# Kernel tuning notes

Measured on AMD Instinct MI355X. Metric: run time of the kernel, lower is better.

The kernel has to match this reference:

```python
import jax, jax.numpy as jnp
import numpy as np

B, LC, LQ, D = 64, 512, 64, 256

def setup_inputs() -> dict:
    key = jax.random.key(0)
    k1, k2, k3, k4 = jax.random.split(key, 4)
    contex = jax.random.normal(k1, (B, LC, D), dtype=jnp.float32)
    question = jax.random.normal(k2, (B, LQ, D), dtype=jnp.float32)
    W_weight = jax.random.normal(k3, (1, 3 * D), dtype=jnp.float32) * (1.0 / np.sqrt(3 * D))
    W_bias = jax.random.normal(k4, (1,), dtype=jnp.float32) * 0.01
    return {"contex": contex, "question": question, "W_weight": W_weight, "W_bias": W_bias}

def reference(contex, question, W_weight, W_bias):
    d = contex.shape[-1]
    w = W_weight[0]  # [3D]; cat order in original is [q, c, q*c]
    wq, wc, wi = w[:d], w[d:2 * d], w[2 * d:]
    # S[b,i,j] = c_i.wc + q_j.wq + (c_i*q_j).wi + bias  (trilinear decomposition)
    s_c = contex @ wc                                   # [B, Lc]
    s_q = question @ wq                                 # [B, Lq]
    s_i = jnp.einsum('bid,bjd->bij', contex * wi, question)  # [B, Lc, Lq]
    S = s_i + s_c[:, :, None] + s_q[:, None, :] + W_bias[0]
    S1 = jax.nn.softmax(S, axis=2)                      # over question
    S2 = jax.nn.softmax(S, axis=1)                      # over context
    A = jnp.einsum('bij,bjd->bid', S1, question)        # [B, Lc, D]
    S3 = jnp.einsum('bij,bkj->bik', S1, S2)             # [B, Lc, Lc]
    Bm = jnp.einsum('bik,bkd->bid', S3, contex)         # [B, Lc, D]
    out = jnp.concatenate([contex, A, contex * A, contex * Bm], axis=2)  # [B, Lc, 4D]
    return out  # dropout is identity at inference
```

## Files before the change

kernel.cpp:

```cpp
#include <hip/hip_runtime.h>
#include <hip/hip_bf16.h>

#define BB 64
#define LCC 512
#define LQQ 64
#define DDD 256

typedef short bf16x8 __attribute__((ext_vector_type(8)));
typedef float f32x4 __attribute__((ext_vector_type(4)));
typedef unsigned u32x4 __attribute__((ext_vector_type(4)));

static __device__ __forceinline__ unsigned pk2bf(float a, float b) {
  __hip_bfloat162 h = __float22bfloat162_rn(make_float2(a, b));
  unsigned u;
  __builtin_memcpy(&u, &h, sizeof(u));
  return u;
}
static __device__ __forceinline__ unsigned short bf1(float f) {
  __hip_bfloat16 h = __float2bfloat16(f);
  unsigned short u;
  __builtin_memcpy(&u, &h, sizeof(u));
  return u;
}

static __device__ __forceinline__ void nt_store4(float* p, float a, float b, float c, float d) {
  f32x4 v = { a, b, c, d };
  __builtin_nontemporal_store(v, (f32x4*)p);
}

__global__ __launch_bounds__(256) void k1_scores(
    const float* __restrict__ cx, const float* __restrict__ qu,
    const float* __restrict__ W, const float* __restrict__ Wb,
    unsigned short* __restrict__ P, unsigned short* __restrict__ Et,
    float* __restrict__ csp)
{
  __shared__ float w_lds[768];
  __shared__ unsigned short Bs[64 * 264];
  __shared__ float E_lds[64 * 65];
  __shared__ float sc_lds[64];
  __shared__ float sq_lds[64];

  const int tid = threadIdx.x;
  const int b    = blockIdx.x >> 3;
  const int tile = blockIdx.x & 7;
  const int i0 = tile * 64;
  const int w = tid >> 6, lane = tid & 63, quad = lane >> 4, ln = lane & 15;

  for (int idx = tid; idx < 768; idx += 256) w_lds[idx] = W[idx];
  __syncthreads();

  {
    const int bj = tid >> 2, bc = tid & 3;
    const float4* src = (const float4*)(qu + ((size_t)(b * LQQ + bj)) * DDD + bc * 64);
    const float* wq = w_lds + bc * 64;
    unsigned short* dst = Bs + bj * 264 + bc * 64;
    float sqp = 0.f;
#pragma unroll
    for (int u = 0; u < 16; ++u) {
      float4 v = src[u];
      sqp += v.x * wq[u*4+0] + v.y * wq[u*4+1] + v.z * wq[u*4+2] + v.w * wq[u*4+3];
      uint2 o = { pk2bf(v.x, v.y), pk2bf(v.z, v.w) };
      *(uint2*)(dst + u * 4) = o;
    }
    sqp += __shfl_xor(sqp, 1);
    sqp += __shfl_xor(sqp, 2);
    if ((tid & 3) == 0) sq_lds[bj] = sqp;
  }
  __syncthreads();

  f32x4 acc[4];
#pragma unroll
  for (int c = 0; c < 4; ++c) acc[c] = (f32x4){0.f, 0.f, 0.f, 0.f};

  float scp = 0.f;
  const float* cxrow = cx + ((size_t)(b * LCC + i0 + w * 16 + ln)) * DDD;
#pragma unroll
  for (int kk = 0; kk < 4; ++kk)
#pragma unroll
    for (int ks = 0; ks < 2; ++ks) {
      const int k0 = kk * 64 + ks * 32 + quad * 8;
      float4 c0 = *(const float4*)(cxrow + k0);
      float4 c1 = *(const float4*)(cxrow + k0 + 4);
      const float* wcp = w_lds + 256 + k0;
      const float* wip = w_lds + 512 + k0;
      scp += c0.x*wcp[0] + c0.y*wcp[1] + c0.z*wcp[2] + c0.w*wcp[3]
           + c1.x*wcp[4] + c1.y*wcp[5] + c1.z*wcp[6] + c1.w*wcp[7];
      u32x4 av = { pk2bf(c0.x * wip[0], c0.y * wip[1]),
                   pk2bf(c0.z * wip[2], c0.w * wip[3]),
                   pk2bf(c1.x * wip[4], c1.y * wip[5]),
                   pk2bf(c1.z * wip[6], c1.w * wip[7]) };
      bf16x8 af;
      __builtin_memcpy(&af, &av, sizeof(af));
#pragma unroll
      for (int tn = 0; tn < 4; ++tn) {
        bf16x8 bf = *(const bf16x8*)(Bs + (tn * 16 + ln) * 264 + k0);
        acc[tn] = __builtin_amdgcn_mfma_f32_16x16x32_bf16(af, bf, acc[tn], 0, 0, 0);
      }
    }

  scp += __shfl_xor(scp, 16);
  scp += __shfl_xor(scp, 32);
  if (lane < 16) sc_lds[w * 16 + ln] = scp + Wb[0];
  __syncthreads();

#pragma unroll
  for (int tn = 0; tn < 4; ++tn)
#pragma unroll
    for (int r = 0; r < 4; ++r) {
      int il = w * 16 + quad * 4 + r;
      int j  = tn * 16 + ln;
      E_lds[il * 65 + j] = __expf(acc[tn][r] + sc_lds[il] + sq_lds[j]);
    }
  __syncthreads();

  {
    const int i = tid >> 2, c = tid & 3;
    const float* srcr = E_lds + i * 65 + c * 16;
    float s = 0.f;
#pragma unroll
    for (int j = 0; j < 16; ++j) s += srcr[j];
    s += __shfl_xor(s, 1);
    s += __shfl_xor(s, 2);
    const float ri = 1.0f / s;
    unsigned short* dst = P + ((size_t)(b * LCC + i0 + i)) * 64 + c * 16;
#pragma unroll
    for (int u = 0; u < 4; ++u) {
      uint2 o = { pk2bf(srcr[u*4+0]*ri, srcr[u*4+1]*ri),
                  pk2bf(srcr[u*4+2]*ri, srcr[u*4+3]*ri) };
      *(uint2*)(dst + u * 4) = o;
    }
  }
  {
    const int j = tid >> 2, c = tid & 3;
    float s = 0.f;
#pragma unroll
    for (int r = 0; r < 16; ++r) s += E_lds[(c * 16 + r) * 65 + j];
    s += __shfl_xor(s, 1);
    s += __shfl_xor(s, 2);
    if ((tid & 3) == 0) csp[((size_t)(b * 8 + tile)) * 64 + j] = s;
  }
  {
    const int j = tid >> 2, c = tid & 3;
    unsigned short* dst = Et + ((size_t)(b * LQQ + j)) * LCC + i0 + c * 16;
#pragma unroll
    for (int u = 0; u < 4; ++u) {
      uint2 o = { pk2bf(E_lds[(c*16 + u*4 + 0) * 65 + j],
                        E_lds[(c*16 + u*4 + 1) * 65 + j]),
                  pk2bf(E_lds[(c*16 + u*4 + 2) * 65 + j],
                        E_lds[(c*16 + u*4 + 3) * 65 + j]) };
      *(uint2*)(dst + u * 4) = o;
    }
  }
}

__global__ __launch_bounds__(256) void k2_tmat(
    const float* __restrict__ cx, const float* __restrict__ qu,
    const unsigned short* __restrict__ Et, const float* __restrict__ csp,
    unsigned short* __restrict__ Qt, unsigned short* __restrict__ Tt)
{
  __shared__ unsigned short Bs2[2][32 * 72];
  __shared__ float Tl[64 * 37];
  __shared__ float csinv[64];

  const int tid = threadIdx.x;
  const int b  = blockIdx.x >> 3;
  const int d0 = (blockIdx.x & 7) * 32;
  const int w = tid >> 6, lane = tid & 63, quad = lane >> 4, ln = lane & 15;

  {
    const int j = tid >> 2, c = tid & 3;
    const float* srow = qu + ((size_t)(b * LQQ + j)) * DDD + d0 + c * 8;
    float4 v0 = *(const float4*)srow;
    float4 v1 = *(const float4*)(srow + 4);
    float* t = Tl + j * 37 + c * 8;
    t[0]=v0.x; t[1]=v0.y; t[2]=v0.z; t[3]=v0.w;
    t[4]=v1.x; t[5]=v1.y; t[6]=v1.z; t[7]=v1.w;
  }
  if (tid < 64) {
    float s = 0.f;
#pragma unroll
    for (int t = 0; t < 8; ++t) s += csp[((size_t)(b * 8 + t)) * 64 + tid];
    csinv[tid] = 1.0f / s;
  }
  __syncthreads();
  {
    const int d = tid >> 3, cj = tid & 7;
    unsigned short* dst = Qt + ((size_t)(b * DDD + d0 + d)) * 64 + cj * 8;
    uint2 o0 = { pk2bf(Tl[(cj*8+0)*37+d], Tl[(cj*8+1)*37+d]),
                 pk2bf(Tl[(cj*8+2)*37+d], Tl[(cj*8+3)*37+d]) };
    uint2 o1 = { pk2bf(Tl[(cj*8+4)*37+d], Tl[(cj*8+5)*37+d]),
                 pk2bf(Tl[(cj*8+6)*37+d], Tl[(cj*8+7)*37+d]) };
    *(uint2*)dst = o0;
    *(uint2*)(dst + 4) = o1;
  }

  f32x4 acc[2];
  acc[0] = (f32x4){0.f, 0.f, 0.f, 0.f};
  acc[1] = (f32x4){0.f, 0.f, 0.f, 0.f};
  const unsigned short* etrow = Et + ((size_t)(b * LQQ + w * 16 + ln)) * LCC;
  const int r2 = tid >> 2, c2 = tid & 3;

  for (int kk = 0; kk < 8; ++kk) {
    unsigned short* bufw = Bs2[kk & 1];
    {
      const float* srow = cx + ((size_t)(b * LCC + kk * 64 + r2)) * DDD + d0 + c2 * 8;
      float4 v0 = *(const float4*)srow;
      float4 v1 = *(const float4*)(srow + 4);
      bufw[(c2*8+0)*72 + r2] = bf1(v0.x);
      bufw[(c2*8+1)*72 + r2] = bf1(v0.y);
      bufw[(c2*8+2)*72 + r2] = bf1(v0.z);
      bufw[(c2*8+3)*72 + r2] = bf1(v0.w);
      bufw[(c2*8+4)*72 + r2] = bf1(v1.x);
      bufw[(c2*8+5)*72 + r2] = bf1(v1.y);
      bufw[(c2*8+6)*72 + r2] = bf1(v1.z);
      bufw[(c2*8+7)*72 + r2] = bf1(v1.w);
    }
    bf16x8 af0 = *(const bf16x8*)(etrow + kk * 64 + quad * 8);
    bf16x8 af1 = *(const bf16x8*)(etrow + kk * 64 + 32 + quad * 8);
    __syncthreads();
    const unsigned short* bufr = Bs2[kk & 1];
#pragma unroll
    for (int tn = 0; tn < 2; ++tn) {
      bf16x8 bf0 = *(const bf16x8*)(bufr + (tn * 16 + ln) * 72 + quad * 8);
      bf16x8 bf1v = *(const bf16x8*)(bufr + (tn * 16 + ln) * 72 + 32 + quad * 8);
      acc[tn] = __builtin_amdgcn_mfma_f32_16x16x32_bf16(af0, bf0, acc[tn], 0, 0, 0);
      acc[tn] = __builtin_amdgcn_mfma_f32_16x16x32_bf16(af1, bf1v, acc[tn], 0, 0, 0);
    }
  }

#pragma unroll
  for (int tn = 0; tn < 2; ++tn)
#pragma unroll
    for (int r = 0; r < 4; ++r) {
      int j = w * 16 + quad * 4 + r;
      Tl[j * 37 + tn * 16 + ln] = acc[tn][r] * csinv[j];
    }
  __syncthreads();
  {
    const int d = tid >> 3, cj = tid & 7;
    unsigned short* dst = Tt + ((size_t)(b * DDD + d0 + d)) * 64 + cj * 8;
    uint2 o0 = { pk2bf(Tl[(cj*8+0)*37+d], Tl[(cj*8+1)*37+d]),
                 pk2bf(Tl[(cj*8+2)*37+d], Tl[(cj*8+3)*37+d]) };
    uint2 o1 = { pk2bf(Tl[(cj*8+4)*37+d], Tl[(cj*8+5)*37+d]),
                 pk2bf(Tl[(cj*8+6)*37+d], Tl[(cj*8+7)*37+d]) };
    *(uint2*)dst = o0;
    *(uint2*)(dst + 4) = o1;
  }
}

__global__ __launch_bounds__(256, 2) void k3_out(
    const float* __restrict__ cx,
    const unsigned short* __restrict__ P,
    const unsigned short* __restrict__ Qt,
    const unsigned short* __restrict__ Tt,
    float* __restrict__ out)
{
  __shared__ float TrA[16 * 260];
  __shared__ float TrB[16 * 260];

  const int tid = threadIdx.x;
  const int b  = blockIdx.x >> 3;
  const int i0 = (blockIdx.x & 7) * 64;
  const int w = tid >> 6, lane = tid & 63, quad = lane >> 4, ln = lane & 15;

  const unsigned short* pbase = P + ((size_t)(b * LCC + i0)) * 64;
  const unsigned short* qbase = Qt + (size_t)b * DDD * 64;
  const unsigned short* tbase = Tt + (size_t)b * DDD * 64;

  f32x4 accA[4][4], accB[4][4];
#pragma unroll
  for (int a = 0; a < 4; ++a)
#pragma unroll
    for (int c = 0; c < 4; ++c) {
      accA[a][c] = (f32x4){0.f, 0.f, 0.f, 0.f};
      accB[a][c] = (f32x4){0.f, 0.f, 0.f, 0.f};
    }

#pragma unroll
  for (int ks = 0; ks < 2; ++ks) {
    bf16x8 af[4];
#pragma unroll
    for (int tm = 0; tm < 4; ++tm)
      af[tm] = *(const bf16x8*)(pbase + (tm * 16 + ln) * 64 + ks * 32 + quad * 8);
#pragma unroll
    for (int tn = 0; tn < 4; ++tn) {
      const size_t boff = ((size_t)(w * 64 + tn * 16 + ln)) * 64 + ks * 32 + quad * 8;
      bf16x8 bq = *(const bf16x8*)(qbase + boff);
      bf16x8 bt = *(const bf16x8*)(tbase + boff);
#pragma unroll
      for (int tm = 0; tm < 4; ++tm) {
        accA[tm][tn] = __builtin_amdgcn_mfma_f32_16x16x32_bf16(af[tm], bq, accA[tm][tn], 0, 0, 0);
        accB[tm][tn] = __builtin_amdgcn_mfma_f32_16x16x32_bf16(af[tm], bt, accB[tm][tn], 0, 0, 0);
      }
    }
  }

  const float* cxb = cx + (size_t)b * LCC * DDD;
  float* ob = out + (size_t)b * LCC * 1024;
  const int row = tid >> 4;
  const int fq  = tid & 15;

#pragma unroll
  for (int tm = 0; tm < 4; ++tm) {
#pragma unroll
    for (int tn = 0; tn < 4; ++tn)
#pragma unroll
      for (int r = 0; r < 4; ++r) {
        int rloc = quad * 4 + r;
        TrA[rloc * 260 + w * 64 + tn * 16 + ln] = accA[tm][tn][r];
        TrB[rloc * 260 + w * 64 + tn * 16 + ln] = accB[tm][tn][r];
      }
    __syncthreads();
    const int i = i0 + tm * 16 + row;
#pragma unroll
    for (int u = 0; u < 4; ++u) {
      int c0 = (fq + u * 16) * 4;
      float4 a  = *(const float4*)(TrA + row * 260 + c0);
      float4 bm = *(const float4*)(TrB + row * 260 + c0);
      float4 c  = *(const float4*)(cxb + (size_t)i * DDD + c0);
      nt_store4(ob + (size_t)i * 1024 + c0,       c.x, c.y, c.z, c.w);
      nt_store4(ob + (size_t)i * 1024 + 256 + c0, a.x, a.y, a.z, a.w);
      nt_store4(ob + (size_t)i * 1024 + 512 + c0, c.x*a.x, c.y*a.y, c.z*a.z, c.w*a.w);
      nt_store4(ob + (size_t)i * 1024 + 768 + c0, c.x*bm.x, c.y*bm.y, c.z*bm.z, c.w*bm.w);
    }
    __syncthreads();
  }
}

extern "C" void kernel_launch(void* const* d_in, const int* in_sizes, int n_in,
                              void* d_out, int out_size, void* d_ws, size_t ws_size,
                              hipStream_t stream) {
  const float* cx = (const float*)d_in[0];
  const float* qu = (const float*)d_in[1];
  const float* W  = (const float*)d_in[2];
  const float* Wb = (const float*)d_in[3];
  float* out = (float*)d_out;

  char* wsb = (char*)d_ws;
  unsigned short* P   = (unsigned short*)(wsb);
  unsigned short* Et  = (unsigned short*)(wsb + (4ull << 20));
  unsigned short* Qt  = (unsigned short*)(wsb + (8ull << 20));
  unsigned short* Tt  = (unsigned short*)(wsb + (10ull << 20));
  float*          csp = (float*)(wsb + (12ull << 20));

  k1_scores<<<dim3(512), dim3(256), 0, stream>>>(cx, qu, W, Wb, P, Et, csp);
  k2_tmat  <<<dim3(512), dim3(256), 0, stream>>>(cx, qu, Et, csp, Qt, Tt);
  k3_out   <<<dim3(512), dim3(256), 0, stream>>>(cx, P, Qt, Tt, out);
}
```

Baseline: 198.7 us.

## Fuse three kernels into one persistent kernel with per-batch atomic counters

Merges the score, T-matrix and output kernels into a single launch in which the 8 blocks of each batch coordinate through global atomic counters, spinning until all 8 peers have finished a stage. Shared memory is reused across the three phases through one byte buffer. This aims to remove two kernel launch gaps and the tail effects between stages, at the cost of a memset launch and spin-waits. Correctness relies on all blocks of a batch being resident at once; the 2-blocks-per-CU bound makes 512 blocks fit on 256 CUs. The wait loop breaks out after a fixed number of iterations instead of deadlocking.

```diff
diff --git a/kernel.cpp b/kernel.cpp
--- a/kernel.cpp
+++ b/kernel.cpp
@@ -28,302 +28,312 @@
   __builtin_nontemporal_store(v, (f32x4*)p);
 }
 
-__global__ __launch_bounds__(256) void k1_scores(
+static __device__ __forceinline__ void signal_cnt(int* c, int tid) {
+  __threadfence();
+  __syncthreads();
+  if (tid == 0)
+    __hip_atomic_fetch_add(c, 1, __ATOMIC_RELEASE, __HIP_MEMORY_SCOPE_AGENT);
+}
+static __device__ __forceinline__ void wait_cnt(int* c, int target) {
+  int n = 0;
+  while (__hip_atomic_load(c, __ATOMIC_ACQUIRE, __HIP_MEMORY_SCOPE_AGENT) < target) {
+    __builtin_amdgcn_s_sleep(8);
+    if (++n > (1 << 20)) break;
+  }
+}
+
+__global__ __launch_bounds__(256, 2) void fused(
     const float* __restrict__ cx, const float* __restrict__ qu,
     const float* __restrict__ W, const float* __restrict__ Wb,
     unsigned short* __restrict__ P, unsigned short* __restrict__ Et,
-    float* __restrict__ csp)
+    float* __restrict__ csp, unsigned short* __restrict__ Qt,
+    unsigned short* __restrict__ Tt, float* __restrict__ out,
+    int* __restrict__ cnt1, int* __restrict__ cnt2)
 {
-  __shared__ float w_lds[768];
-  __shared__ unsigned short Bs[64 * 264];
-  __shared__ float E_lds[64 * 65];
-  __shared__ float sc_lds[64];
-  __shared__ float sq_lds[64];
+  __shared__ __align__(16) char smem[54016];
 
   const int tid = threadIdx.x;
-  const int b    = blockIdx.x >> 3;
-  const int tile = blockIdx.x & 7;
-  const int i0 = tile * 64;
+  const int b = blockIdx.x >> 3;
+  const int s = blockIdx.x & 7;
   const int w = tid >> 6, lane = tid & 63, quad = lane >> 4, ln = lane & 15;
 
-  for (int idx = tid; idx < 768; idx += 256) w_lds[idx] = W[idx];
-  __syncthreads();
-
   {
-    const int bj = tid >> 2, bc = tid & 3;
-    const float4* src = (const float4*)(qu + ((size_t)(b * LQQ + bj)) * DDD + bc * 64);
-    const float* wq = w_lds + bc * 64;
-    unsigned short* dst = Bs + bj * 264 + bc * 64;
-    float sqp = 0.f;
-#pragma unroll
-    for (int u = 0; u < 16; ++u) {
-      float4 v = src[u];
-      sqp += v.x * wq[u*4+0] + v.y * wq[u*4+1] + v.z * wq[u*4+2] + v.w * wq[u*4+3];
-      uint2 o = { pk2bf(v.x, v.y), pk2bf(v.z, v.w) };
-      *(uint2*)(dst + u * 4) = o;
-    }
-    sqp += __shfl_xor(sqp, 1);
-    sqp += __shfl_xor(sqp, 2);
-    if ((tid & 3) == 0) sq_lds[bj] = sqp;
+    float* w_lds          = (float*)(smem);
+    unsigned short* Bs    = (unsigned short*)(smem + 3072);
+    float* E_lds          = (float*)(smem + 36864);
+    float* sc_lds         = (float*)(smem + 53504);
+    float* sq_lds         = (float*)(smem + 53760);
+    const int i0 = s * 64;
+
+    for (int idx = tid; idx < 768; idx += 256) w_lds[idx] = W[idx];
+    __syncthreads();
+
+    {
+      const int bj = tid >> 2, bc = tid & 3;
+      const float4* src = (const float4*)(qu + ((size_t)(b * LQQ + bj)) * DDD + bc * 64);
+      const float* wq = w_lds + bc * 64;
+      unsigned short* dst = Bs + bj * 264 + bc * 64;
+      float sqp = 0.f;
+#pragma unroll
+      for (int u = 0; u < 16; ++u) {
+        float4 v = src[u];
+        sqp += v.x * wq[u*4+0] + v.y * wq[u*4+1] + v.z * wq[u*4+2] + v.w * wq[u*4+3];
+        uint2 o = { pk2bf(v.x, v.y), pk2bf(v.z, v.w) };
+        *(uint2*)(dst + u * 4) = o;
+      }
+      sqp += __shfl_xor(sqp, 1);
+      sqp += __shfl_xor(sqp, 2);
+      if ((tid & 3) == 0) sq_lds[bj] = sqp;
+    }
+    __syncthreads();
+
+    f32x4 acc[4];
+#pragma unroll
+    for (int c = 0; c < 4; ++c) acc[c] = (f32x4){0.f, 0.f, 0.f, 0.f};
+
+    float scp = 0.f;
+    const float* cxrow = cx + ((size_t)(b * LCC + i0 + w * 16 + ln)) * DDD;
+#pragma unroll
+    for (int kk = 0; kk < 4; ++kk)
+#pragma unroll
+      for (int ks = 0; ks < 2; ++ks) {
+        const int k0 = kk * 64 + ks * 32 + quad * 8;
+        float4 c0 = *(const float4*)(cxrow + k0);
+        float4 c1 = *(const float4*)(cxrow + k0 + 4);
+        const float* wcp = w_lds + 256 + k0;
+        const float* wip = w_lds + 512 + k0;
+        scp += c0.x*wcp[0] + c0.y*wcp[1] + c0.z*wcp[2] + c0.w*wcp[3]
+             + c1.x*wcp[4] + c1.y*wcp[5] + c1.z*wcp[6] + c1.w*wcp[7];
+        u32x4 av = { pk2bf(c0.x * wip[0], c0.y * wip[1]),
+                     pk2bf(c0.z * wip[2], c0.w * wip[3]),
+                     pk2bf(c1.x * wip[4], c1.y * wip[5]),
+                     pk2bf(c1.z * wip[6], c1.w * wip[7]) };
+        bf16x8 af;
+        __builtin_memcpy(&af, &av, sizeof(af));
+#pragma unroll
+        for (int tn = 0; tn < 4; ++tn) {
+          bf16x8 bf = *(const bf16x8*)(Bs + (tn * 16 + ln) * 264 + k0);
+          acc[tn] = __builtin_amdgcn_mfma_f32_16x16x32_bf16(af, bf, acc[tn], 0, 0, 0);
+        }
+      }
+
+    scp += __shfl_xor(scp, 16);
+    scp += __shfl_xor(scp, 32);
+    if (lane < 16) sc_lds[w * 16 + ln] = scp + Wb[0];
+    __syncthreads();
+
+#pragma unroll
+    for (int tn = 0; tn < 4; ++tn)
+#pragma unroll
+      for (int r = 0; r < 4; ++r) {
+        int il = w * 16 + quad * 4 + r;
+        int j  = tn * 16 + ln;
+        E_lds[il * 65 + j] = __expf(acc[tn][r] + sc_lds[il] + sq_lds[j]);
+      }
+    __syncthreads();
+
+    {
+      const int i = tid >> 2, c = tid & 3;
+      const float* srcr = E_lds + i * 65 + c * 16;
+      float sum = 0.f;
+#pragma unroll
+      for (int j = 0; j < 16; ++j) sum += srcr[j];
+      sum += __shfl_xor(sum, 1);
+      sum += __shfl_xor(sum, 2);
+      const float ri = 1.0f / sum;
+      unsigned short* dst = P + ((size_t)(b * LCC + i0 + i)) * 64 + c * 16;
+#pragma unroll
+      for (int u = 0; u < 4; ++u) {
+        uint2 o = { pk2bf(srcr[u*4+0]*ri, srcr[u*4+1]*ri),
+                    pk2bf(srcr[u*4+2]*ri, srcr[u*4+3]*ri) };
+        *(uint2*)(dst + u * 4) = o;
+      }
+    }
+    {
+      const int j = tid >> 2, c = tid & 3;
+      float sum = 0.f;
+#pragma unroll
+      for (int r = 0; r < 16; ++r) sum += E_lds[(c * 16 + r) * 65 + j];
+      sum += __shfl_xor(sum, 1);
+      sum += __shfl_xor(sum, 2);
+      if ((tid & 3) == 0) csp[((size_t)(b * 8 + s)) * 64 + j] = sum;
+    }
+    {
+      const int j = tid >> 2, c = tid & 3;
+      unsigned short* dst = Et + ((size_t)(b * LQQ + j)) * LCC + i0 + c * 16;
+#pragma unroll
+      for (int u = 0; u < 4; ++u) {
+        uint2 o = { pk2bf(E_lds[(c*16 + u*4 + 0) * 65 + j],
+                          E_lds[(c*16 + u*4 + 1) * 65 + j]),
+                    pk2bf(E_lds[(c*16 + u*4 + 2) * 65 + j],
+                          E_lds[(c*16 + u*4 + 3) * 65 + j]) };
+        *(uint2*)(dst + u * 4) = o;
+      }
+    }
   }
-  __syncthreads();
-
-  f32x4 acc[4];
-#pragma unroll
-  for (int c = 0; c < 4; ++c) acc[c] = (f32x4){0.f, 0.f, 0.f, 0.f};
-
-  float scp = 0.f;
-  const float* cxrow = cx + ((size_t)(b * LCC + i0 + w * 16 + ln)) * DDD;
-#pragma unroll
-  for (int kk = 0; kk < 4; ++kk)
-#pragma unroll
-    for (int ks = 0; ks < 2; ++ks) {
-      const int k0 = kk * 64 + ks * 32 + quad * 8;
-      float4 c0 = *(const float4*)(cxrow + k0);
-      float4 c1 = *(const float4*)(cxrow + k0 + 4);
-      const float* wcp = w_lds + 256 + k0;
-      const float* wip = w_lds + 512 + k0;
-      scp += c0.x*wcp[0] + c0.y*wcp[1] + c0.z*wcp[2] + c0.w*wcp[3]
-           + c1.x*wcp[4] + c1.y*wcp[5] + c1.z*wcp[6] + c1.w*wcp[7];
-      u32x4 av = { pk2bf(c0.x * wip[0], c0.y * wip[1]),
-                   pk2bf(c0.z * wip[2], c0.w * wip[3]),
-                   pk2bf(c1.x * wip[4], c1.y * wip[5]),
-                   pk2bf(c1.z * wip[6], c1.w * wip[7]) };
-      bf16x8 af;
-      __builtin_memcpy(&af, &av, sizeof(af));
-#pragma unroll
-      for (int tn = 0; tn < 4; ++tn) {
-        bf16x8 bf = *(const bf16x8*)(Bs + (tn * 16 + ln) * 264 + k0);
-        acc[tn] = __builtin_amdgcn_mfma_f32_16x16x32_bf16(af, bf, acc[tn], 0, 0, 0);
-      }
-    }
-
-  scp += __shfl_xor(scp, 16);
-  scp += __shfl_xor(scp, 32);
-  if (lane < 16) sc_lds[w * 16 + ln] = scp + Wb[0];
-  __syncthreads();
-
-#pragma unroll
-  for (int tn = 0; tn < 4; ++tn)
-#pragma unroll
-    for (int r = 0; r < 4; ++r) {
-      int il = w * 16 + quad * 4 + r;
-      int j  = tn * 16 + ln;
-      E_lds[il * 65 + j] = __expf(acc[tn][r] + sc_lds[il] + sq_lds[j]);
-    }
-  __syncthreads();
+
+  signal_cnt(&cnt1[b], tid);
 
   {
-    const int i = tid >> 2, c = tid & 3;
-    const float* srcr = E_lds + i * 65 + c * 16;
-    float s = 0.f;
-#pragma unroll
-    for (int j = 0; j < 16; ++j) s += srcr[j];
-    s += __shfl_xor(s, 1);
-    s += __shfl_xor(s, 2);
-    const float ri = 1.0f / s;
-    unsigned short* dst = P + ((size_t)(b * LCC + i0 + i)) * 64 + c * 16;
-#pragma unroll
-    for (int u = 0; u < 4; ++u) {
-      uint2 o = { pk2bf(srcr[u*4+0]*ri, srcr[u*4+1]*ri),
-                  pk2bf(srcr[u*4+2]*ri, srcr[u*4+3]*ri) };
-      *(uint2*)(dst + u * 4) = o;
-    }
-  }
-  {
-    const int j = tid >> 2, c = tid & 3;
-    float s = 0.f;
-#pragma unroll
-    for (int r = 0; r < 16; ++r) s += E_lds[(c * 16 + r) * 65 + j];
-    s += __shfl_xor(s, 1);
-    s += __shfl_xor(s, 2);
-    if ((tid & 3) == 0) csp[((size_t)(b * 8 + tile)) * 64 + j] = s;
-  }
-  {
-    const int j = tid >> 2, c = tid & 3;
-    unsigned short* dst = Et + ((size_t)(b * LQQ + j)) * LCC + i0 + c * 16;
-#pragma unroll
-    for (int u = 0; u < 4; ++u) {
-      uint2 o = { pk2bf(E_lds[(c*16 + u*4 + 0) * 65 + j],
-                        E_lds[(c*16 + u*4 + 1) * 65 + j]),
-                  pk2bf(E_lds[(c*16 + u*4 + 2) * 65 + j],
-                        E_lds[(c*16 + u*4 + 3) * 65 + j]) };
-      *(uint2*)(dst + u * 4) = o;
-    }
-  }
-}
-
-__global__ __launch_bounds__(256) void k2_tmat(
-    const float* __restrict__ cx, const float* __restrict__ qu,
-    const unsigned short* __restrict__ Et, const float* __restrict__ csp,
-    unsigned short* __restrict__ Qt, unsigned short* __restrict__ Tt)
-{
-  __shared__ unsigned short Bs2[2][32 * 72];
-  __shared__ float Tl[64 * 37];
-  __shared__ float csinv[64];
-
-  const int tid = threadIdx.x;
-  const int b  = blockIdx.x >> 3;
-  const int d0 = (blockIdx.x & 7) * 32;
-  const int w = tid >> 6, lane = tid & 63, quad = lane >> 4, ln = lane & 15;
-
-  {
-    const int j = tid >> 2, c = tid & 3;
-    const float* srow = qu + ((size_t)(b * LQQ + j)) * DDD + d0 + c * 8;
-    float4 v0 = *(const float4*)srow;
-    float4 v1 = *(const float4*)(srow + 4);
-    float* t = Tl + j * 37 + c * 8;
-    t[0]=v0.x; t[1]=v0.y; t[2]=v0.z; t[3]=v0.w;
-    t[4]=v1.x; t[5]=v1.y; t[6]=v1.z; t[7]=v1.w;
-  }
-  if (tid < 64) {
-    float s = 0.f;
-#pragma unroll
-    for (int t = 0; t < 8; ++t) s += csp[((size_t)(b * 8 + t)) * 64 + tid];
-    csinv[tid] = 1.0f / s;
-  }
-  __syncthreads();
-  {
-    const int d = tid >> 3, cj = tid & 7;
-    unsigned short* dst = Qt + ((size_t)(b * DDD + d0 + d)) * 64 + cj * 8;
-    uint2 o0 = { pk2bf(Tl[(cj*8+0)*37+d], Tl[(cj*8+1)*37+d]),
-                 pk2bf(Tl[(cj*8+2)*37+d], Tl[(cj*8+3)*37+d]) };
-    uint2 o1 = { pk2bf(Tl[(cj*8+4)*37+d], Tl[(cj*8+5)*37+d]),
-                 pk2bf(Tl[(cj*8+6)*37+d], Tl[(cj*8+7)*37+d]) };
-    *(uint2*)dst = o0;
-    *(uint2*)(dst + 4) = o1;
-  }
-
-  f32x4 acc[2];
-  acc[0] = (f32x4){0.f, 0.f, 0.f, 0.f};
-  acc[1] = (f32x4){0.f, 0.f, 0.f, 0.f};
-  const unsigned short* etrow = Et + ((size_t)(b * LQQ + w * 16 + ln)) * LCC;
-  const int r2 = tid >> 2, c2 = tid & 3;
-
-  for (int kk = 0; kk < 8; ++kk) {
-    unsigned short* bufw = Bs2[kk & 1];
-    {
-      const float* srow = cx + ((size_t)(b * LCC + kk * 64 + r2)) * DDD + d0 + c2 * 8;
+    unsigned short* Bs2 = (unsigned short*)(smem);
+    float* Tl           = (float*)(smem + 9216);
+    float* csinv        = (float*)(smem + 18688);
+    const int d0 = s * 32;
+
+    {
+      const int j = tid >> 2, c = tid & 3;
+      const float* srow = qu + ((size_t)(b * LQQ + j)) * DDD + d0 + c * 8;
       float4 v0 = *(const float4*)srow;
       float4 v1 = *(const float4*)(srow + 4);
-      bufw[(c2*8+0)*72 + r2] = bf1(v0.x);
-      bufw[(c2*8+1)*72 + r2] = bf1(v0.y);
-      bufw[(c2*8+2)*72 + r2] = bf1(v0.z);
-      bufw[(c2*8+3)*72 + r2] = bf1(v0.w);
-      bufw[(c2*8+4)*72 + r2] = bf1(v1.x);
-      bufw[(c2*8+5)*72 + r2] = bf1(v1.y);
-      bufw[(c2*8+6)*72 + r2] = bf1(v1.z);
-      bufw[(c2*8+7)*72 + r2] = bf1(v1.w);
-    }
-    bf16x8 af0 = *(const bf16x8*)(etrow + kk * 64 + quad * 8);
-    bf16x8 af1 = *(const bf16x8*)(etrow + kk * 64 + 32 + quad * 8);
-    __syncthreads();
-    const unsigned short* bufr = Bs2[kk & 1];
-#pragma unroll
-    for (int tn = 0; tn < 2; ++tn) {
-      bf16x8 bf0 = *(const bf16x8*)(bufr + (tn * 16 + ln) * 72 + quad * 8);
-      bf16x8 bf1v = *(const bf16x8*)(bufr + (tn * 16 + ln) * 72 + 32 + quad * 8);
-      acc[tn] = __builtin_amdgcn_mfma_f32_16x16x32_bf16(af0, bf0, acc[tn], 0, 0, 0);
-      acc[tn] = __builtin_amdgcn_mfma_f32_16x16x32_bf16(af1, bf1v, acc[tn], 0, 0, 0);
+      float* t = Tl + j * 37 + c * 8;
+      t[0]=v0.x; t[1]=v0.y; t[2]=v0.z; t[3]=v0.w;
+      t[4]=v1.x; t[5]=v1.y; t[6]=v1.z; t[7]=v1.w;
+    }
+    if (tid == 0) wait_cnt(&cnt1[b], 8);
+    __syncthreads();
+
+    {
+      const int d = tid >> 3, cj = tid & 7;
+      unsigned short* dst = Qt + ((size_t)(b * DDD + d0 + d)) * 64 + cj * 8;
+      uint2 o0 = { pk2bf(Tl[(cj*8+0)*37+d], Tl[(cj*8+1)*37+d]),
+                   pk2bf(Tl[(cj*8+2)*37+d], Tl[(cj*8+3)*37+d]) };
+      uint2 o1 = { pk2bf(Tl[(cj*8+4)*37+d], Tl[(cj*8+5)*37+d]),
+                   pk2bf(Tl[(cj*8+6)*37+d], Tl[(cj*8+7)*37+d]) };
+      *(uint2*)dst = o0;
+      *(uint2*)(dst + 4) = o1;
+    }
+    if (tid < 64) {
+      float sum = 0.f;
+#pragma unroll
+      for (int t = 0; t < 8; ++t) sum += csp[((size_t)(b * 8 + t)) * 64 + tid];
+      csinv[tid] = 1.0f / sum;
+    }
+
+    f32x4 acc[2];
+    acc[0] = (f32x4){0.f, 0.f, 0.f, 0.f};
+    acc[1] = (f32x4){0.f, 0.f, 0.f, 0.f};
+    const unsigned short* etrow = Et + ((size_t)(b * LQQ + w * 16 + ln)) * LCC;
+    const int r2 = tid >> 2, c2 = tid & 3;
+
+    for (int kk = 0; kk < 8; ++kk) {
+      unsigned short* bufw = Bs2 + (kk & 1) * 2304;
+      {
+        const float* srow = cx + ((size_t)(b * LCC + kk * 64 + r2)) * DDD + d0 + c2 * 8;
+        float4 v0 = *(const float4*)srow;
+        float4 v1 = *(const float4*)(srow + 4);
+        bufw[(c2*8+0)*72 + r2] = bf1(v0.x);
+        bufw[(c2*8+1)*72 + r2] = bf1(v0.y);
+        bufw[(c2*8+2)*72 + r2] = bf1(v0.z);
+        bufw[(c2*8+3)*72 + r2] = bf1(v0.w);
+        bufw[(c2*8+4)*72 + r2] = bf1(v1.x);
+        bufw[(c2*8+5)*72 + r2] = bf1(v1.y);
+        bufw[(c2*8+6)*72 + r2] = bf1(v1.z);
+        bufw[(c2*8+7)*72 + r2] = bf1(v1.w);
+      }
+      bf16x8 af0 = *(const bf16x8*)(etrow + kk * 64 + quad * 8);
+      bf16x8 af1 = *(const bf16x8*)(etrow + kk * 64 + 32 + quad * 8);
+      __syncthreads();
+      const unsigned short* bufr = Bs2 + (kk & 1) * 2304;
+#pragma unroll
+      for (int tn = 0; tn < 2; ++tn) {
+        bf16x8 bf0  = *(const bf16x8*)(bufr + (tn * 16 + ln) * 72 + quad * 8);
+        bf16x8 bf1v = *(const bf16x8*)(bufr + (tn * 16 + ln) * 72 + 32 + quad * 8);
+        acc[tn] = __builtin_amdgcn_mfma_f32_16x16x32_bf16(af0, bf0, acc[tn], 0, 0, 0);
+        acc[tn] = __builtin_amdgcn_mfma_f32_16x16x32_bf16(af1, bf1v, acc[tn], 0, 0, 0);
+      }
+    }
+
+#pragma unroll
+    for (int tn = 0; tn < 2; ++tn)
+#pragma unroll
+      for (int r = 0; r < 4; ++r) {
+        int j = w * 16 + quad * 4 + r;
+        Tl[j * 37 + tn * 16 + ln] = acc[tn][r] * csinv[j];
+      }
+    __syncthreads();
+    {
+      const int d = tid >> 3, cj = tid & 7;
+      unsigned short* dst = Tt + ((size_t)(b * DDD + d0 + d)) * 64 + cj * 8;
+      uint2 o0 = { pk2bf(Tl[(cj*8+0)*37+d], Tl[(cj*8+1)*37+d]),
+                   pk2bf(Tl[(cj*8+2)*37+d], Tl[(cj*8+3)*37+d]) };
+      uint2 o1 = { pk2bf(Tl[(cj*8+4)*37+d], Tl[(cj*8+5)*37+d]),
+                   pk2bf(Tl[(cj*8+6)*37+d], Tl[(cj*8+7)*37+d]) };
+      *(uint2*)dst = o0;
+      *(uint2*)(dst + 4) = o1;
     }
   }
 
-#pragma unroll
-  for (int tn = 0; tn < 2; ++tn)
-#pragma unroll
-    for (int r = 0; r < 4; ++r) {
-      int j = w * 16 + quad * 4 + r;
-      Tl[j * 37 + tn * 16 + ln] = acc[tn][r] * csinv[j];
-    }
+  signal_cnt(&cnt2[b], tid);
+  if (tid == 0) wait_cnt(&cnt2[b], 8);
   __syncthreads();
+
   {
-    const int d = tid >> 3, cj = tid & 7;
-    unsigned short* dst = Tt + ((size_t)(b * DDD + d0 + d)) * 64 + cj * 8;
-    uint2 o0 = { pk2bf(Tl[(cj*8+0)*37+d], Tl[(cj*8+1)*37+d]),
-                 pk2bf(Tl[(cj*8+2)*37+d], Tl[(cj*8+3)*37+d]) };
-    uint2 o1 = { pk2bf(Tl[(cj*8+4)*37+d], Tl[(cj*8+5)*37+d]),
-                 pk2bf(Tl[(cj*8+6)*37+d], Tl[(cj*8+7)*37+d]) };
-    *(uint2*)dst = o0;
-    *(uint2*)(dst + 4) = o1;
-  }
-}
-
-__global__ __launch_bounds__(256, 2) void k3_out(
-    const float* __restrict__ cx,
-    const unsigned short* __restrict__ P,
-    const unsigned short* __restrict__ Qt,
-    const unsigned short* __restrict__ Tt,
-    float* __restrict__ out)
-{
-  __shared__ float TrA[16 * 260];
-  __shared__ float TrB[16 * 260];
-
-  const int tid = threadIdx.x;
-  const int b  = blockIdx.x >> 3;
-  const int i0 = (blockIdx.x & 7) * 64;
-  const int w = tid >> 6, lane = tid & 63, quad = lane >> 4, ln = lane & 15;
-
-  const unsigned short* pbase = P + ((size_t)(b * LCC + i0)) * 64;
-  const unsigned short* qbase = Qt + (size_t)b * DDD * 64;
-  const unsigned short* tbase = Tt + (size_t)b * DDD * 64;
-
-  f32x4 accA[4][4], accB[4][4];
-#pragma unroll
-  for (int a = 0; a < 4; ++a)
-#pragma unroll
-    for (int c = 0; c < 4; ++c) {
-      accA[a][c] = (f32x4){0.f, 0.f, 0.f, 0.f};
-      accB[a][c] = (f32x4){0.f, 0.f, 0.f, 0.f};
-    }
-
-#pragma unroll
-  for (int ks = 0; ks < 2; ++ks) {
-    bf16x8 af[4];
-#pragma unroll
-    for (int tm = 0; tm < 4; ++tm)
-      af[tm] = *(const bf16x8*)(pbase + (tm * 16 + ln) * 64 + ks * 32 + quad * 8);
-#pragma unroll
-    for (int tn = 0; tn < 4; ++tn) {
-      const size_t boff = ((size_t)(w * 64 + tn * 16 + ln)) * 64 + ks * 32 + quad * 8;
-      bf16x8 bq = *(const bf16x8*)(qbase + boff);
-      bf16x8 bt = *(const bf16x8*)(tbase + boff);
-#pragma unroll
-      for (int tm = 0; tm < 4; ++tm) {
-        accA[tm][tn] = __builtin_amdgcn_mfma_f32_16x16x32_bf16(af[tm], bq, accA[tm][tn], 0, 0, 0);
-        accB[tm][tn] = __builtin_amdgcn_mfma_f32_16x16x32_bf16(af[tm], bt, accB[tm][tn], 0, 0, 0);
-      }
-    }
-  }
-
-  const float* cxb = cx + (size_t)b * LCC * DDD;
-  float* ob = out + (size_t)b * LCC * 1024;
-  const int row = tid >> 4;
-  const int fq  = tid & 15;
-
-#pragma unroll
-  for (int tm = 0; tm < 4; ++tm) {
-#pragma unroll
-    for (int tn = 0; tn < 4; ++tn)
-#pragma unroll
-      for (int r = 0; r < 4; ++r) {
-        int rloc = quad * 4 + r;
-        TrA[rloc * 260 + w * 64 + tn * 16 + ln] = accA[tm][tn][r];
-        TrB[rloc * 260 + w * 64 + tn * 16 + ln] = accB[tm][tn][r];
-      }
-    __syncthreads();
-    const int i = i0 + tm * 16 + row;
-#pragma unroll
-    for (int u = 0; u < 4; ++u) {
-      int c0 = (fq + u * 16) * 4;
-      float4 a  = *(const float4*)(TrA + row * 260 + c0);
-      float4 bm = *(const float4*)(TrB + row * 260 + c0);
-      float4 c  = *(const float4*)(cxb + (size_t)i * DDD + c0);
-      nt_store4(ob + (size_t)i * 1024 + c0,       c.x, c.y, c.z, c.w);
-      nt_store4(ob + (size_t)i * 1024 + 256 + c0, a.x, a.y, a.z, a.w);
-      nt_store4(ob + (size_t)i * 1024 + 512 + c0, c.x*a.x, c.y*a.y, c.z*a.z, c.w*a.w);
-      nt_store4(ob + (size_t)i * 1024 + 768 + c0, c.x*bm.x, c.y*bm.y, c.z*bm.z, c.w*bm.w);
-    }
-    __syncthreads();
+    float* TrA = (float*)(smem);
+    float* TrB = (float*)(smem + 16640);
+    const int i0 = s * 64;
+
+    const unsigned short* pbase = P + ((size_t)(b * LCC + i0)) * 64;
+    const unsigned short* qbase = Qt + (size_t)b * DDD * 64;
+    const unsigned short* tbase = Tt + (size_t)b * DDD * 64;
+
+    f32x4 accA[4][4], accB[4][4];
+#pragma unroll
+    for (int a = 0; a < 4; ++a)
+#pragma unroll
+      for (int c = 0; c < 4; ++c) {
+        accA[a][c] = (f32x4){0.f, 0.f, 0.f, 0.f};
+        accB[a][c] = (f32x4){0.f, 0.f, 0.f, 0.f};
+      }
+
+#pragma unroll
+    for (int ks = 0; ks < 2; ++ks) {
+      bf16x8 af[4];
+#pragma unroll
+      for (int tm = 0; tm < 4; ++tm)
+        af[tm] = *(const bf16x8*)(pbase + (tm * 16 + ln) * 64 + ks * 32 + quad * 8);
+#pragma unroll
+      for (int tn = 0; tn < 4; ++tn) {
+        const size_t boff = ((size_t)(w * 64 + tn * 16 + ln)) * 64 + ks * 32 + quad * 8;
+        bf16x8 bq = *(const bf16x8*)(qbase + boff);
+        bf16x8 bt = *(const bf16x8*)(tbase + boff);
+#pragma unroll
+        for (int tm = 0; tm < 4; ++tm) {
+          accA[tm][tn] = __builtin_amdgcn_mfma_f32_16x16x32_bf16(af[tm], bq, accA[tm][tn], 0, 0, 0);
+          accB[tm][tn] = __builtin_amdgcn_mfma_f32_16x16x32_bf16(af[tm], bt, accB[tm][tn], 0, 0, 0);
+        }
+      }
+    }
+
+    const float* cxb = cx + (size_t)b * LCC * DDD;
+    float* ob = out + (size_t)b * LCC * 1024;
+    const int row = tid >> 4;
+    const int fq  = tid & 15;
+
+#pragma unroll
+    for (int tm = 0; tm < 4; ++tm) {
+#pragma unroll
+      for (int tn = 0; tn < 4; ++tn)
+#pragma unroll
+        for (int r = 0; r < 4; ++r) {
+          int rloc = quad * 4 + r;
+          TrA[rloc * 260 + w * 64 + tn * 16 + ln] = accA[tm][tn][r];
+          TrB[rloc * 260 + w * 64 + tn * 16 + ln] = accB[tm][tn][r];
+        }
+      __syncthreads();
+      const int i = i0 + tm * 16 + row;
+#pragma unroll
+      for (int u = 0; u < 4; ++u) {
+        int c0 = (fq + u * 16) * 4;
+        float4 a  = *(const float4*)(TrA + row * 260 + c0);
+        float4 bm = *(const float4*)(TrB + row * 260 + c0);
+        float4 c  = *(const float4*)(cxb + (size_t)i * DDD + c0);
+        nt_store4(ob + (size_t)i * 1024 + c0,       c.x, c.y, c.z, c.w);
+        nt_store4(ob + (size_t)i * 1024 + 256 + c0, a.x, a.y, a.z, a.w);
+        nt_store4(ob + (size_t)i * 1024 + 512 + c0, c.x*a.x, c.y*a.y, c.z*a.z, c.w*a.w);
+        nt_store4(ob + (size_t)i * 1024 + 768 + c0, c.x*bm.x, c.y*bm.y, c.z*bm.z, c.w*bm.w);
+      }
+      __syncthreads();
+    }
   }
 }
 
@@ -342,8 +352,9 @@
   unsigned short* Qt  = (unsigned short*)(wsb + (8ull << 20));
   unsigned short* Tt  = (unsigned short*)(wsb + (10ull << 20));
   float*          csp = (float*)(wsb + (12ull << 20));
-
-  k1_scores<<<dim3(512), dim3(256), 0, stream>>>(cx, qu, W, Wb, P, Et, csp);
-  k2_tmat  <<<dim3(512), dim3(256), 0, stream>>>(cx, qu, Et, csp, Qt, Tt);
-  k3_out   <<<dim3(512), dim3(256), 0, stream>>>(cx, P, Qt, Tt, out);
-}
+  int*            cnt = (int*)(wsb + (13ull << 20));
+
+  hipMemsetAsync(cnt, 0, 512, stream);
+  fused<<<dim3(512), dim3(256), 0, stream>>>(cx, qu, W, Wb, P, Et, csp, Qt, Tt,
+                                             out, cnt, cnt + 64);
+}
```

Result: slower. 402.2 us (+102.5%).
